# Kernel tuning notes

Hardware: AMD Instinct MI355X
Metric: run time of the kernel (lower is better)

## Reference

```python
import jax, jax.numpy as jnp
import numpy as np

B, S, D = 2, 2048, 1024
H, DK, DV = 16, 64, 64

def setup_inputs() -> dict:
    key = jax.random.key(0)
    ks = jax.random.split(key, 5)
    scale = 1.0 / np.sqrt(D)  # xavier-ish
    return {
        "Q": jax.random.normal(ks[0], (B, S, D), dtype=jnp.float32),
        "attn_mask": jax.random.uniform(ks[1], (B, S), dtype=jnp.float32),
        "W_Q": jax.random.normal(ks[2], (H * DK, D), dtype=jnp.float32) * scale,
        "b_Q": jnp.zeros((H * DK,), dtype=jnp.float32),
        "W_K": jax.random.normal(ks[3], (H * DK, D), dtype=jnp.float32) * scale,
        "b_K": jnp.zeros((H * DK,), dtype=jnp.float32),
        "W_V": jax.random.normal(ks[4], (H * DV, D), dtype=jnp.float32) * scale,
        "b_V": jnp.zeros((H * DV,), dtype=jnp.float32),
    }

def reference(Q, attn_mask, W_Q, b_Q, W_K, b_K, W_V, b_V):
    b, s, _ = Q.shape
    # projections -> [B, H, S, d]
    q = (Q @ W_Q.T + b_Q).reshape(b, s, H, DK).transpose(0, 2, 1, 3)
    k = (Q @ W_K.T + b_K).reshape(b, s, H, DK).transpose(0, 2, 1, 3)
    v = (Q @ W_V.T + b_V).reshape(b, s, H, DV).transpose(0, 2, 1, 3)
    # exp-based attention (NOT stable softmax), multiplicative mask
    scores = jnp.einsum('bhqd,bhkd->bhqk', q, k) / np.sqrt(DK)
    scores = jnp.exp(scores)
    # mask [B, S_key] broadcast over heads and queries -> [B, 1, 1, S]
    scores = scores * attn_mask[:, None, None, :]
    attn = scores / (jnp.sum(scores, axis=-1, keepdims=True) + 1e-8)
    context = jnp.einsum('bhqk,bhkd->bhqd', attn, v)
    # [B, H, S, DV] -> [B, S, H*DV]
    return context.transpose(0, 2, 1, 3).reshape(b, s, H * DV)
```

## Files before the change

### kernel.cpp

```cpp
#include <hip/hip_runtime.h>
#include <hip/hip_bf16.h>
#include <math.h>

#define BATCH  2
#define S_LEN  2048
#define DMODEL 1024
#define NH     16
#define DHEAD  64

typedef __attribute__((ext_vector_type(8))) short bf16x8;
typedef __attribute__((ext_vector_type(4))) float f32x4;

#define MFMA16(a,b,c) __builtin_amdgcn_mfma_f32_16x16x32_bf16((a),(b),(c),0,0,0)

#define QSCALE 0.18033688011110793f
#define EXP2F(x) __builtin_amdgcn_exp2f(x)

__device__ __forceinline__ unsigned int pkbf(float a, float b) {
    __hip_bfloat162 h = __float22bfloat162_rn(make_float2(a, b));
    union { __hip_bfloat162 h; unsigned int u; } v; v.h = h; return v.u;
}
__device__ __forceinline__ void gl2lds16(const void* g, void* l) {
    __builtin_amdgcn_global_load_lds(
        (const __attribute__((address_space(1))) void*)(g),
        (__attribute__((address_space(3))) void*)(l), 16, 0, 0);
}

__global__ __launch_bounds__(256) void cvt_all(
    const float* __restrict__ Q,  const float* __restrict__ WQ,
    const float* __restrict__ WK, const float* __restrict__ WV,
    const float* __restrict__ msk,
    unsigned short* __restrict__ Qbf, unsigned short* __restrict__ Wbf,
    unsigned short* __restrict__ mbf)
{
    int i = blockIdx.x * blockDim.x + threadIdx.x;
    const float* src;
    unsigned short* dst;
    int off;
    if (i < 524288) {
        src = Q; dst = Qbf; off = i;
    } else if (i < 917504) {
        int j = i - 524288;
        int which = j >> 17;
        src = (which == 0) ? WQ : ((which == 1) ? WK : WV);
        dst = Wbf + ((size_t)which << 20);
        off = j & 131071;
    } else {
        int j = i - 917504;
        if (j >= 512) return;
        src = msk; dst = mbf; off = j;
    }
    float4 a = ((const float4*)src)[2*off];
    float4 b = ((const float4*)src)[2*off + 1];
    uint4 o;
    o.x = pkbf(a.x, a.y); o.y = pkbf(a.z, a.w);
    o.z = pkbf(b.x, b.y); o.w = pkbf(b.z, b.w);
    ((uint4*)dst)[off] = o;
}

__global__ __launch_bounds__(256) void proj_mfma(
    const unsigned short* __restrict__ Abf,
    const unsigned short* __restrict__ Wbf,
    const float* __restrict__ bQ, const float* __restrict__ bK,
    const float* __restrict__ bV, const float* __restrict__ mask,
    unsigned short* __restrict__ qw, unsigned short* __restrict__ kw,
    unsigned short* __restrict__ vt)
{
    __shared__ union {
        struct { unsigned short At[2][128*64]; unsigned short Bt[2][128*64]; } s;
        unsigned short Ct[128*132];
    } sm;

    const int tid  = threadIdx.x;
    const int lane = tid & 63;
    const int wv   = tid >> 6;
    const int wm   = (wv >> 1) * 64;
    const int wn   = (wv & 1) * 64;
    const int q15  = lane & 15;
    const int quad = lane >> 4;

    const int f  = blockIdx.x + (blockIdx.y << 3) + (blockIdx.z << 8);
    const int l  = (f & 7) * 96 + (f >> 3);
    const int z  = l >> 8;
    const int lr = l & 255;
    const int n0 = (lr & 7) * 128;
    const int m0 = (lr >> 3) * 128;

    const unsigned short* Wz = Wbf + (size_t)z * DMODEL * DMODEL;
    const float* bias = (z == 0) ? bQ : ((z == 1) ? bK : bV);

    f32x4 zero4 = {0.f, 0.f, 0.f, 0.f};
    f32x4 acc[4][4];
    #pragma unroll
    for (int i = 0; i < 4; ++i)
        #pragma unroll
        for (int j = 0; j < 4; ++j) acc[i][j] = zero4;

    #define STAGE_PROJ(BUF, K0)                                                \
        _Pragma("unroll")                                                      \
        for (int c = 0; c < 4; ++c) {                                          \
            int o   = tid * 16 + c * 4096;                                     \
            int row = o >> 7;                                                  \
            int lb  = (o & 127) ^ ((row & 7) << 4);                            \
            gl2lds16(Abf + (size_t)(m0 + row) * DMODEL + (K0) + (lb >> 1),     \
                     (char*)sm.s.At[BUF] + o);                                 \
            gl2lds16(Wz  + (size_t)(n0 + row) * DMODEL + (K0) + (lb >> 1),     \
                     (char*)sm.s.Bt[BUF] + o);                                 \
        }

    STAGE_PROJ(0, 0)
    __syncthreads();

    const int sw = (q15 & 7) << 4;

    for (int t = 0; t < 16; ++t) {
        const int buf = t & 1;
        if (t < 15) { STAGE_PROJ(buf ^ 1, (t + 1) * 64) }

        bf16x8 af[4][2], bfr[4][2];
        #pragma unroll
        for (int i = 0; i < 4; ++i) {
            const char* pa = (const char*)sm.s.At[buf] + (wm + i*16 + q15) * 128;
            const char* pb = (const char*)sm.s.Bt[buf] + (wn + i*16 + q15) * 128;
            af[i][0]  = *(const bf16x8*)(pa + (( 0 + quad*16) ^ sw));
            af[i][1]  = *(const bf16x8*)(pa + ((64 + quad*16) ^ sw));
            bfr[i][0] = *(const bf16x8*)(pb + (( 0 + quad*16) ^ sw));
            bfr[i][1] = *(const bf16x8*)(pb + ((64 + quad*16) ^ sw));
        }

        if (z < 2) {
            #pragma unroll
            for (int ks = 0; ks < 2; ++ks)
                #pragma unroll
                for (int i = 0; i < 4; ++i)
                    #pragma unroll
                    for (int j = 0; j < 4; ++j)
                        acc[i][j] = MFMA16(bfr[j][ks], af[i][ks], acc[i][j]);
        } else {
            #pragma unroll
            for (int ks = 0; ks < 2; ++ks)
                #pragma unroll
                for (int i = 0; i < 4; ++i)
                    #pragma unroll
                    for (int j = 0; j < 4; ++j)
                        acc[i][j] = MFMA16(af[i][ks], bfr[j][ks], acc[i][j]);
        }
        __syncthreads();
    }
    #undef STAGE_PROJ

    if (z < 2) {
        const float qs = (z == 0) ? QSCALE : 1.0f;
        #pragma unroll
        for (int i = 0; i < 4; ++i) {
            int ml = wm + i*16 + q15;
            #pragma unroll
            for (int j = 0; j < 4; ++j) {
                int nl = wn + j*16 + quad*4;
                float4 b4 = *(const float4*)(bias + n0 + nl);
                f32x4 v = acc[i][j];
                uint2 u;
                u.x = pkbf((v.x + b4.x)*qs, (v.y + b4.y)*qs);
                u.y = pkbf((v.z + b4.z)*qs, (v.w + b4.w)*qs);
                *(uint2*)&sm.Ct[ml*132 + nl] = u;
            }
        }
    } else {
        #pragma unroll
        for (int i = 0; i < 4; ++i) {
            int ml = wm + i*16 + quad*4;
            int sg = m0 + ml;
            int b2 = sg >> 11, s0g = sg & 2047;
            float4 mk4 = *(const float4*)(mask + (size_t)b2*S_LEN + s0g);
            #pragma unroll
            for (int j = 0; j < 4; ++j) {
                int nl = wn + j*16 + q15;
                float bv = bias[n0 + nl];
                f32x4 v = acc[i][j];
                uint2 u;
                u.x = pkbf((v.x + bv)*mk4.x, (v.y + bv)*mk4.y);
                u.y = pkbf((v.z + bv)*mk4.z, (v.w + bv)*mk4.w);
                *(uint2*)&sm.Ct[nl*132 + ml] = u;
            }
        }
    }
    __syncthreads();

    {
        int row  = tid >> 1;
        int half = (tid & 1) * 64;
        const uint4* src = (const uint4*)&sm.Ct[row*132 + half];
        unsigned short* dst;
        if (z < 2) {
            unsigned short* outp = (z == 0) ? qw : kw;
            int mg = m0 + row;  int b2 = mg >> 11, s = mg & 2047;
            int n  = n0 + half; int hh = n >> 6;
            dst = outp + (((size_t)b2*NH + hh)*S_LEN + s)*DHEAD;
        } else {
            int n  = n0 + row;  int hh = n >> 6, dv = n & 63;
            int b2 = m0 >> 11, s0 = m0 & 2047;
            dst = vt + (((size_t)b2*NH + hh)*DHEAD + dv)*S_LEN + s0 + half;
        }
        #pragma unroll
        for (int c = 0; c < 8; ++c) ((uint4*)dst)[c] = src[c];
    }
}

__global__ __launch_bounds__(256, 2) void attn_mfma(
    const unsigned short* __restrict__ qw, const unsigned short* __restrict__ kw,
    const unsigned short* __restrict__ vt, const unsigned short* __restrict__ mbf,
    float* __restrict__ out)
{
    __shared__ __align__(16) unsigned short Ks[2][64][72];
    __shared__ __align__(16) unsigned short Vs[2][64][72];

    const int tid  = threadIdx.x;
    const int lane = tid & 63;
    const int wv   = tid >> 6;
    const int q15  = lane & 15;
    const int quad = lane >> 4;

    const int orig = blockIdx.x + (blockIdx.y << 4) + (blockIdx.z << 8);
    const int lid  = (orig & 7) * 64 + (orig >> 3);
    const int q0   = (lid & 15) * 128;
    const int head = lid >> 4;
    const int h    = head & 15;
    const int b    = head >> 4;

    const size_t headoff = ((size_t)b * NH + h) * S_LEN * DHEAD;
    const unsigned short* qb = qw + headoff;
    const unsigned short* kb = kw + headoff;
    const unsigned short* vb = vt + headoff;
    const unsigned short* mb = mbf + (size_t)b * S_LEN;

    bf16x8 qf[2][2];
    #pragma unroll
    for (int qi = 0; qi < 2; ++qi) {
        const unsigned short* qr = qb + (size_t)(q0 + wv*32 + qi*16 + q15)*DHEAD;
        qf[qi][0] = *(const bf16x8*)(qr + quad*8);
        qf[qi][1] = *(const bf16x8*)(qr + 32 + quad*8);
    }

    const int srow = tid >> 3;
    const int scol = (tid & 7) * 8;
    const int prow = ((srow >> 2) & 1) * 16 + ((srow >> 3) & 3) * 4 + (srow & 3);

    f32x4 zero4 = {0.f, 0.f, 0.f, 0.f};
    f32x4 oacc[2][4];
    f32x4 dacc[2];
    #pragma unroll
    for (int qi = 0; qi < 2; ++qi) {
        dacc[qi] = zero4;
        #pragma unroll
        for (int nj = 0; nj < 4; ++nj) oacc[qi][nj] = zero4;
    }

    uint4 kr0, kr1, vr0, vr1;
    kr0 = *(const uint4*)(kb + (size_t)(srow)     *DHEAD + scol);
    kr1 = *(const uint4*)(kb + (size_t)(srow + 32)*DHEAD + scol);
    vr0 = *(const uint4*)(vb + (size_t)(srow)     *S_LEN + scol);
    vr1 = *(const uint4*)(vb + (size_t)(srow + 32)*S_LEN + scol);
    bf16x8 mc0 = *(const bf16x8*)(mb + quad*8);
    bf16x8 mc1 = *(const bf16x8*)(mb + 32 + quad*8);

    for (int t = 0; t < 32; ++t) {
        const int buf = t & 1;
        const int k0  = t * 64;
        *(uint4*)&Ks[buf][prow][scol]      = kr0;
        *(uint4*)&Ks[buf][prow + 32][scol] = kr1;
        *(uint4*)&Vs[buf][srow][scol]      = vr0;
        *(uint4*)&Vs[buf][srow + 32][scol] = vr1;
        const int kn = (t < 31) ? k0 + 64 : 0;
        kr0 = *(const uint4*)(kb + (size_t)(kn + srow)     *DHEAD + scol);
        kr1 = *(const uint4*)(kb + (size_t)(kn + srow + 32)*DHEAD + scol);
        vr0 = *(const uint4*)(vb + (size_t)(srow)     *S_LEN + kn + scol);
        vr1 = *(const uint4*)(vb + (size_t)(srow + 32)*S_LEN + kn + scol);
        bf16x8 mn0 = *(const bf16x8*)(mb + kn + quad*8);
        bf16x8 mn1 = *(const bf16x8*)(mb + kn + 32 + quad*8);
        __syncthreads();

        f32x4 s[2][4];
        __builtin_amdgcn_s_setprio(1);
        #pragma unroll
        for (int ks = 0; ks < 4; ++ks) {
            bf16x8 kf0 = *(const bf16x8*)&Ks[buf][ks*16 + q15][quad*8];
            bf16x8 kf1 = *(const bf16x8*)&Ks[buf][ks*16 + q15][32 + quad*8];
            #pragma unroll
            for (int qi = 0; qi < 2; ++qi) {
                f32x4 a = MFMA16(kf0, qf[qi][0], zero4);
                s[qi][ks] = MFMA16(kf1, qf[qi][1], a);
            }
        }
        __builtin_amdgcn_s_setprio(0);
        bf16x8 pf[2][2];
        #pragma unroll
        for (int qi = 0; qi < 2; ++qi) {
            uint4 u0, u1;
            u0.x = pkbf(EXP2F(s[qi][0][0]), EXP2F(s[qi][0][1]));
            u0.y = pkbf(EXP2F(s[qi][0][2]), EXP2F(s[qi][0][3]));
            u0.z = pkbf(EXP2F(s[qi][1][0]), EXP2F(s[qi][1][1]));
            u0.w = pkbf(EXP2F(s[qi][1][2]), EXP2F(s[qi][1][3]));
            u1.x = pkbf(EXP2F(s[qi][2][0]), EXP2F(s[qi][2][1]));
            u1.y = pkbf(EXP2F(s[qi][2][2]), EXP2F(s[qi][2][3]));
            u1.z = pkbf(EXP2F(s[qi][3][0]), EXP2F(s[qi][3][1]));
            u1.w = pkbf(EXP2F(s[qi][3][2]), EXP2F(s[qi][3][3]));
            union { uint4 u; bf16x8 h; } c0, c1;
            c0.u = u0; c1.u = u1;
            pf[qi][0] = c0.h;
            pf[qi][1] = c1.h;
        }
        __builtin_amdgcn_s_setprio(1);
        #pragma unroll
        for (int qi = 0; qi < 2; ++qi) {
            dacc[qi] = MFMA16(pf[qi][0], mc0, dacc[qi]);
            dacc[qi] = MFMA16(pf[qi][1], mc1, dacc[qi]);
        }
        #pragma unroll
        for (int nj = 0; nj < 4; ++nj) {
            bf16x8 vf0 = *(const bf16x8*)&Vs[buf][nj*16 + q15][quad*8];
            bf16x8 vf1 = *(const bf16x8*)&Vs[buf][nj*16 + q15][32 + quad*8];
            #pragma unroll
            for (int qi = 0; qi < 2; ++qi) {
                oacc[qi][nj] = MFMA16(pf[qi][0], vf0, oacc[qi][nj]);
                oacc[qi][nj] = MFMA16(pf[qi][1], vf1, oacc[qi][nj]);
            }
        }
        __builtin_amdgcn_s_setprio(0);
        mc0 = mn0; mc1 = mn1;
    }

    #pragma unroll
    for (int qi = 0; qi < 2; ++qi)
        #pragma unroll
        for (int r = 0; r < 4; ++r) {
            float inv = 1.0f / (dacc[qi][r] + 1e-8f);
            size_t row = ((size_t)b*S_LEN + q0 + wv*32 + qi*16 + quad*4 + r)*DMODEL
                       + h*DHEAD;
            #pragma unroll
            for (int nj = 0; nj < 4; ++nj)
                out[row + nj*16 + q15] = oacc[qi][nj][r] * inv;
        }
}

extern "C" void kernel_launch(void* const* d_in, const int* in_sizes, int n_in,
                              void* d_out, int out_size, void* d_ws, size_t ws_size,
                              hipStream_t stream) {
    const float* Q    = (const float*)d_in[0];
    const float* msk  = (const float*)d_in[1];
    const float* W_Q  = (const float*)d_in[2];
    const float* b_Q  = (const float*)d_in[3];
    const float* W_K  = (const float*)d_in[4];
    const float* b_K  = (const float*)d_in[5];
    const float* W_V  = (const float*)d_in[6];
    const float* b_V  = (const float*)d_in[7];
    float* out = (float*)d_out;

    unsigned short* wsu = (unsigned short*)d_ws;
    unsigned short* Qbf = wsu;
    unsigned short* Wbf = Qbf + (size_t)4096*1024;
    unsigned short* qwb = Wbf + (size_t)3*1024*1024;
    unsigned short* kwb = qwb + (size_t)4*1024*1024;
    unsigned short* vtb = kwb + (size_t)4*1024*1024;
    unsigned short* mbf = vtb + (size_t)4*1024*1024;

    cvt_all<<<3586, 256, 0, stream>>>(Q, W_Q, W_K, W_V, msk, Qbf, Wbf, mbf);

    proj_mfma<<<dim3(8, 32, 3), 256, 0, stream>>>(
        Qbf, Wbf, b_Q, b_K, b_V, msk, qwb, kwb, vtb);

    attn_mfma<<<dim3(S_LEN/128, NH, BATCH), 256, 0, stream>>>(
        qwb, kwb, vtb, mbf, out);
}
```

Baseline: 164.7 us.

## Load K via direct global-to-LDS with XOR swizzle, read V straight to registers

K tiles now go from global memory straight into LDS through global_load_lds, using an XOR-swizzled layout without padding in place of the padded staging array. V tiles skip LDS and are read directly from global memory into MFMA operand registers for each wave. The aim is to cut the register staging, the LDS writes and the LDS footprint. In exchange, every wave reloads V from global/L2 (redundant traffic across the four waves), and the next-tile K prefetch now sits after the barrier.

```diff
diff --git a/kernel.cpp b/kernel.cpp
--- a/kernel.cpp
+++ b/kernel.cpp
@@ -211,8 +211,7 @@
     const unsigned short* __restrict__ vt, const unsigned short* __restrict__ mbf,
     float* __restrict__ out)
 {
-    __shared__ __align__(16) unsigned short Ks[2][64][72];
-    __shared__ __align__(16) unsigned short Vs[2][64][72];
+    __shared__ __align__(16) unsigned short Ks[2][64][64];
 
     const int tid  = threadIdx.x;
     const int lane = tid & 63;
@@ -242,8 +241,17 @@
     }
 
     const int srow = tid >> 3;
-    const int scol = (tid & 7) * 8;
-    const int prow = ((srow >> 2) & 1) * 16 + ((srow >> 3) & 3) * 4 + (srow & 3);
+    const int kap  = (srow & 3) | (((srow >> 4) & 1) << 2) | (((srow >> 2) & 3) << 3);
+    const int lb   = ((tid & 7) * 16) ^ ((srow & 7) << 4);
+    const unsigned short* ksrc0 = kb + (size_t)kap       * DHEAD + (lb >> 1);
+    const unsigned short* ksrc1 = kb + (size_t)(kap + 32)* DHEAD + (lb >> 1);
+    char* kdst0 = (char*)&Ks[0][0][0] + tid * 16;
+    const int sw = (q15 & 7) << 4;
+
+    const unsigned short* vrow[4];
+    #pragma unroll
+    for (int nj = 0; nj < 4; ++nj)
+        vrow[nj] = vb + (size_t)(nj*16 + q15) * S_LEN + quad*8;
 
     f32x4 zero4 = {0.f, 0.f, 0.f, 0.f};
     f32x4 oacc[2][4];
@@ -255,36 +263,39 @@
         for (int nj = 0; nj < 4; ++nj) oacc[qi][nj] = zero4;
     }
 
-    uint4 kr0, kr1, vr0, vr1;
-    kr0 = *(const uint4*)(kb + (size_t)(srow)     *DHEAD + scol);
-    kr1 = *(const uint4*)(kb + (size_t)(srow + 32)*DHEAD + scol);
-    vr0 = *(const uint4*)(vb + (size_t)(srow)     *S_LEN + scol);
-    vr1 = *(const uint4*)(vb + (size_t)(srow + 32)*S_LEN + scol);
+    gl2lds16(ksrc0, kdst0);
+    gl2lds16(ksrc1, kdst0 + 4096);
     bf16x8 mc0 = *(const bf16x8*)(mb + quad*8);
     bf16x8 mc1 = *(const bf16x8*)(mb + 32 + quad*8);
 
     for (int t = 0; t < 32; ++t) {
         const int buf = t & 1;
         const int k0  = t * 64;
-        *(uint4*)&Ks[buf][prow][scol]      = kr0;
-        *(uint4*)&Ks[buf][prow + 32][scol] = kr1;
-        *(uint4*)&Vs[buf][srow][scol]      = vr0;
-        *(uint4*)&Vs[buf][srow + 32][scol] = vr1;
-        const int kn = (t < 31) ? k0 + 64 : 0;
-        kr0 = *(const uint4*)(kb + (size_t)(kn + srow)     *DHEAD + scol);
-        kr1 = *(const uint4*)(kb + (size_t)(kn + srow + 32)*DHEAD + scol);
-        vr0 = *(const uint4*)(vb + (size_t)(srow)     *S_LEN + kn + scol);
-        vr1 = *(const uint4*)(vb + (size_t)(srow + 32)*S_LEN + kn + scol);
+        const int kn  = (t < 31) ? k0 + 64 : 0;
+
+        __syncthreads();
+
+        bf16x8 vf[4][2];
+        #pragma unroll
+        for (int nj = 0; nj < 4; ++nj) {
+            vf[nj][0] = *(const bf16x8*)(vrow[nj] + k0);
+            vf[nj][1] = *(const bf16x8*)(vrow[nj] + k0 + 32);
+        }
+        if (t < 31) {
+            gl2lds16(ksrc0 + (size_t)kn * DHEAD, kdst0 + (buf ^ 1) * 8192);
+            gl2lds16(ksrc1 + (size_t)kn * DHEAD, kdst0 + (buf ^ 1) * 8192 + 4096);
+        }
         bf16x8 mn0 = *(const bf16x8*)(mb + kn + quad*8);
         bf16x8 mn1 = *(const bf16x8*)(mb + kn + 32 + quad*8);
-        __syncthreads();
-
+
+        const char* kbase = (const char*)&Ks[0][0][0] + buf * 8192;
         f32x4 s[2][4];
         __builtin_amdgcn_s_setprio(1);
         #pragma unroll
         for (int ks = 0; ks < 4; ++ks) {
-            bf16x8 kf0 = *(const bf16x8*)&Ks[buf][ks*16 + q15][quad*8];
-            bf16x8 kf1 = *(const bf16x8*)&Ks[buf][ks*16 + q15][32 + quad*8];
+            const char* krp = kbase + (ks*16 + q15) * 128;
+            bf16x8 kf0 = *(const bf16x8*)(krp + (( 0 + quad*16) ^ sw));
+            bf16x8 kf1 = *(const bf16x8*)(krp + ((64 + quad*16) ^ sw));
             #pragma unroll
             for (int qi = 0; qi < 2; ++qi) {
                 f32x4 a = MFMA16(kf0, qf[qi][0], zero4);
@@ -317,12 +328,10 @@
         }
         #pragma unroll
         for (int nj = 0; nj < 4; ++nj) {
-            bf16x8 vf0 = *(const bf16x8*)&Vs[buf][nj*16 + q15][quad*8];
-            bf16x8 vf1 = *(const bf16x8*)&Vs[buf][nj*16 + q15][32 + quad*8];
             #pragma unroll
             for (int qi = 0; qi < 2; ++qi) {
-                oacc[qi][nj] = MFMA16(pf[qi][0], vf0, oacc[qi][nj]);
-                oacc[qi][nj] = MFMA16(pf[qi][1], vf1, oacc[qi][nj]);
+                oacc[qi][nj] = MFMA16(pf[qi][0], vf[nj][0], oacc[qi][nj]);
+                oacc[qi][nj] = MFMA16(pf[qi][1], vf[nj][1], oacc[qi][nj]);
             }
         }
         __builtin_amdgcn_s_setprio(0);
```

After: 189.0 us. 1.15x slower.
